# Kernel optimization log

Measured on AMD Instinct MI355X. Metric: run time of the kernel, lower is better.

The kernel has to match this reference:

```python
import jax, jax.numpy as jnp
import numpy as np

N_NODES = 100000
N_EDGES = 1200000
D_IN = 64
HID = 64
N_CLASSES = 3
N_GRAPHS = 128


def setup_inputs() -> dict:
    key = jax.random.key(0)
    ks = jax.random.split(key, 16)
    def lin(k, fan_in, fan_out):
        s = 1.0 / np.sqrt(fan_in)
        return jax.random.uniform(k, (fan_in, fan_out), jnp.float32, -s, s)
    x = jax.random.normal(ks[0], (N_NODES, D_IN), jnp.float32)
    edge_index = jax.random.randint(ks[1], (2, N_EDGES), 0, N_NODES, jnp.int64 if jax.config.jax_enable_x64 else jnp.int32).astype(jnp.int32)
    batch = jnp.sort(jax.random.randint(ks[2], (N_NODES,), 0, N_GRAPHS).astype(jnp.int32))
    return {
        "x": x,
        "edge_index": edge_index,
        "batch": batch,
        # GraphConv l: out = segment_sum(x[src]) @ Wr + br + x @ Ws  (lin_rel has bias, lin_root no bias)
        "Wr1": lin(ks[3], D_IN, HID), "br1": jnp.zeros((HID,), jnp.float32), "Ws1": lin(ks[4], D_IN, HID),
        "Wr2": lin(ks[5], HID, HID), "br2": jnp.zeros((HID,), jnp.float32), "Ws2": lin(ks[6], HID, HID),
        "Wr3": lin(ks[7], HID, HID), "br3": jnp.zeros((HID,), jnp.float32), "Ws3": lin(ks[8], HID, HID),
        "W_fc1": lin(ks[9], HID, HID), "b_fc1": jnp.zeros((HID,), jnp.float32),
        "W_fc2": lin(ks[10], HID, N_CLASSES), "b_fc2": jnp.zeros((N_CLASSES,), jnp.float32),
    }


def _graph_conv(x, src, dst, Wr, br, Ws):
    # gather -> scatter-add aggregate -> two linear transforms (PyG GraphConv, aggr='add')
    agg = jax.ops.segment_sum(x[src], dst, num_segments=N_NODES)  # [N, d]
    return agg @ Wr + br + x @ Ws


def reference(x, edge_index, batch, Wr1, br1, Ws1, Wr2, br2, Ws2, Wr3, br3, Ws3, W_fc1, b_fc1, W_fc2, b_fc2):
    src, dst = edge_index[0], edge_index[1]
    h = jax.nn.relu(_graph_conv(x, src, dst, Wr1, br1, Ws1))  # dropout is identity at inference
    h = jax.nn.relu(_graph_conv(h, src, dst, Wr2, br2, Ws2))
    h = jax.nn.relu(_graph_conv(h, src, dst, Wr3, br3, Ws3))
    g = jax.ops.segment_sum(h, batch, num_segments=N_GRAPHS)  # global_add_pool -> [G, H]
    g = jax.nn.relu(g @ W_fc1 + b_fc1)
    logits = g @ W_fc2 + b_fc2
    return jax.nn.log_softmax(logits, axis=-1)
```

## Files before the change

kernel.cpp:

```cpp
#include <hip/hip_runtime.h>

#define N_NODES   100000
#define N_EDGES   1200000
#define D         64
#define N_GRAPHS  128
#define N_CLASSES 3

#define TILE      64
#define NTILES    ((N_NODES + TILE - 1) / TILE)
#define TCAP      1024
#define ASTRIDE   72

#define EPB       8192
#define NEB       ((N_EDGES + EPB - 1) / EPB)
#define GRID_PB   1024

typedef unsigned int  uint;
typedef unsigned short ushort;
typedef __attribute__((ext_vector_type(8))) short bf16x8;
typedef __attribute__((ext_vector_type(4))) float f32x4;

__device__ __forceinline__ ushort bf16_rne(float f) {
    uint u = __float_as_uint(f);
    u += 0x7FFFu + ((u >> 16) & 1u);
    return (ushort)(u >> 16);
}
__device__ __forceinline__ float bf16f(ushort h) {
    return __uint_as_float((uint)h << 16);
}
__device__ __forceinline__ void acc8(float* a, uint4 v) {
    a[0] += __uint_as_float(v.x << 16);
    a[1] += __uint_as_float(v.x & 0xFFFF0000u);
    a[2] += __uint_as_float(v.y << 16);
    a[3] += __uint_as_float(v.y & 0xFFFF0000u);
    a[4] += __uint_as_float(v.z << 16);
    a[5] += __uint_as_float(v.z & 0xFFFF0000u);
    a[6] += __uint_as_float(v.w << 16);
    a[7] += __uint_as_float(v.w & 0xFFFF0000u);
}

template<typename PT>
__device__ __forceinline__ void gather_idx(
        float* acc, PT cp, int len,
        const ushort* __restrict__ hin, int fq8) {
    int j = 0;
    for (; j + 8 <= len; j += 8) {
        int s0 = cp[j + 0], s1 = cp[j + 1], s2 = cp[j + 2], s3 = cp[j + 3];
        int s4 = cp[j + 4], s5 = cp[j + 5], s6 = cp[j + 6], s7 = cp[j + 7];
        uint4 v0 = *(const uint4*)(hin + (size_t)s0 * D + fq8);
        uint4 v1 = *(const uint4*)(hin + (size_t)s1 * D + fq8);
        uint4 v2 = *(const uint4*)(hin + (size_t)s2 * D + fq8);
        uint4 v3 = *(const uint4*)(hin + (size_t)s3 * D + fq8);
        uint4 v4 = *(const uint4*)(hin + (size_t)s4 * D + fq8);
        uint4 v5 = *(const uint4*)(hin + (size_t)s5 * D + fq8);
        uint4 v6 = *(const uint4*)(hin + (size_t)s6 * D + fq8);
        uint4 v7 = *(const uint4*)(hin + (size_t)s7 * D + fq8);
        acc8(acc, v0); acc8(acc, v1); acc8(acc, v2); acc8(acc, v3);
        acc8(acc, v4); acc8(acc, v5); acc8(acc, v6); acc8(acc, v7);
    }
    for (; j + 4 <= len; j += 4) {
        int s0 = cp[j + 0], s1 = cp[j + 1], s2 = cp[j + 2], s3 = cp[j + 3];
        uint4 v0 = *(const uint4*)(hin + (size_t)s0 * D + fq8);
        uint4 v1 = *(const uint4*)(hin + (size_t)s1 * D + fq8);
        uint4 v2 = *(const uint4*)(hin + (size_t)s2 * D + fq8);
        uint4 v3 = *(const uint4*)(hin + (size_t)s3 * D + fq8);
        acc8(acc, v0); acc8(acc, v1); acc8(acc, v2); acc8(acc, v3);
    }
    for (; j < len; ++j) {
        uint4 v = *(const uint4*)(hin + (size_t)cp[j] * D + fq8);
        acc8(acc, v);
    }
}

__device__ __forceinline__ void store_agg_bf16(ushort* aggB, int ln, int fq8, const float* acc) {
    uint4 o;
    o.x = (uint)bf16_rne(acc[0]) | ((uint)bf16_rne(acc[1]) << 16);
    o.y = (uint)bf16_rne(acc[2]) | ((uint)bf16_rne(acc[3]) << 16);
    o.z = (uint)bf16_rne(acc[4]) | ((uint)bf16_rne(acc[5]) << 16);
    o.w = (uint)bf16_rne(acc[6]) | ((uint)bf16_rne(acc[7]) << 16);
    *(uint4*)&aggB[ln * ASTRIDE + fq8] = o;
}

__device__ __forceinline__ void mfma_gemm(
        const ushort* __restrict__ hin,
        const ushort* aggB,
        const ushort* __restrict__ Bp,
        int node0, int tid, f32x4* acc) {
    const int lane = tid & 63;
    const int w    = tid >> 6;
    const int r16  = lane & 15;
    const int khi  = lane >> 4;
#pragma unroll
    for (int mt = 0; mt < 4; ++mt) acc[mt] = (f32x4){0.f, 0.f, 0.f, 0.f};
    const ushort* bp = Bp + (w * 64 + lane) * 8;
#pragma unroll
    for (int st = 0; st < 4; ++st) {
        bf16x8 bhi = *(const bf16x8*)(bp + (2 * st    ) * 2048);
        bf16x8 blo = *(const bf16x8*)(bp + (2 * st + 1) * 2048);
        if (st < 2) {
#pragma unroll
            for (int mt = 0; mt < 4; ++mt) {
                bf16x8 a = *(const bf16x8*)(aggB + (16 * mt + r16) * ASTRIDE + st * 32 + khi * 8);
                acc[mt] = __builtin_amdgcn_mfma_f32_16x16x32_bf16(a, bhi, acc[mt], 0, 0, 0);
                acc[mt] = __builtin_amdgcn_mfma_f32_16x16x32_bf16(a, blo, acc[mt], 0, 0, 0);
            }
        } else {
#pragma unroll
            for (int mt = 0; mt < 4; ++mt) {
                bf16x8 a = *(const bf16x8*)(hin + (size_t)(node0 + 16 * mt + r16) * D
                                                + (st - 2) * 32 + khi * 8);
                acc[mt] = __builtin_amdgcn_mfma_f32_16x16x32_bf16(a, bhi, acc[mt], 0, 0, 0);
                acc[mt] = __builtin_amdgcn_mfma_f32_16x16x32_bf16(a, blo, acc[mt], 0, 0, 0);
            }
        }
    }
}

__global__ __launch_bounds__(256) void prep_binA_kernel(
        const float* __restrict__ x, ushort* __restrict__ Xb,
        const int* __restrict__ src, const int* __restrict__ dst,
        int* __restrict__ gcur, int* __restrict__ cbuf,
        const float* __restrict__ Wr1, const float* __restrict__ Ws1,
        const float* __restrict__ Wr2, const float* __restrict__ Ws2,
        const float* __restrict__ Wr3, const float* __restrict__ Ws3,
        ushort* __restrict__ Bp) {
    __shared__ int hist[NTILES];
    __shared__ int pos[NTILES];
    const int tid = threadIdx.x;
    const int bid = blockIdx.x;

    if (bid < NEB) {
        const int e0 = bid * EPB;
        int e1 = e0 + EPB; if (e1 > N_EDGES) e1 = N_EDGES;
        for (int i = tid; i < NTILES; i += 256) hist[i] = 0;
        __syncthreads();
        for (int e = e0 + tid; e < e1; e += 256)
            atomicAdd(&hist[dst[e] >> 6], 1);
        __syncthreads();
        for (int b = tid; b < NTILES; b += 256)
            pos[b] = hist[b] ? atomicAdd(&gcur[b], hist[b]) : 0;
        __syncthreads();
        for (int e = e0 + tid; e < e1; e += 256) {
            int d = dst[e];
            int b = d >> 6;
            int r = atomicAdd(&pos[b], 1);
            if (r < TCAP) cbuf[b * TCAP + r] = src[e] | ((d & 63) << 17);
        }
    } else {
        const int cb  = bid - NEB;
        const int NCB = GRID_PB - NEB;
        const int nodeF4 = N_NODES * D / 4;
        for (int i = cb * 256 + tid; i < nodeF4; i += NCB * 256) {
            float4 v = ((const float4*)x)[i];
            ushort4 o;
            o.x = bf16_rne(v.x); o.y = bf16_rne(v.y);
            o.z = bf16_rne(v.z); o.w = bf16_rne(v.w);
            ((ushort4*)Xb)[i] = o;
        }
        for (int it = cb * 256 + tid; it < 3 * 8 * 4 * 64; it += NCB * 256) {
            int l  = it & 63;
            int w  = (it >> 6) & 3;
            int kt = (it >> 8) & 7;
            int ly = it >> 11;
            int st = kt >> 1;
            int col = w * 16 + (l & 15);
            int kb  = (st & 1) * 32 + (l >> 4) * 8;
            const float* W = (st < 2) ? (ly == 0 ? Wr1 : ly == 1 ? Wr2 : Wr3)
                                      : (ly == 0 ? Ws1 : ly == 1 ? Ws2 : Ws3);
            ushort o[8];
#pragma unroll
            for (int j = 0; j < 8; ++j) {
                float v = W[(kb + j) * D + col];
                ushort h = bf16_rne(v);
                if (kt & 1) {
                    float r = v - bf16f(h);
                    h = bf16_rne(r);
                }
                o[j] = h;
            }
            uint4 u;
            u.x = (uint)o[0] | ((uint)o[1] << 16);
            u.y = (uint)o[2] | ((uint)o[3] << 16);
            u.z = (uint)o[4] | ((uint)o[5] << 16);
            u.w = (uint)o[6] | ((uint)o[7] << 16);
            *(uint4*)(Bp + (size_t)ly * 16384 + ((kt * 4 + w) * 64 + l) * 8) = u;
        }
    }
}

__global__ __launch_bounds__(256, 6) void layer1_fused_kernel(
        const ushort* __restrict__ hin,
        const int* __restrict__ gcur,
        const int* __restrict__ cbuf,
        int* __restrict__ csr,
        int2* __restrict__ rptr2,
        const ushort* __restrict__ Bp,
        const float* __restrict__ br,
        ushort* __restrict__ hout) {
    __shared__ int    ebuf[TCAP];
    __shared__ int    sortedS[TCAP];
    __shared__ ushort aggB[TILE * ASTRIDE];
    __shared__ int    ldeg[TILE];
    __shared__ int    lbeg[TILE];
    __shared__ int    lcur[TILE];

    const int tid   = threadIdx.x;
    const int tile  = blockIdx.x;
    const int base  = tile * TCAP;
    const int node0 = tile * TILE;

    int E = gcur[tile]; if (E > TCAP) E = TCAP;
    if (tid < TILE) ldeg[tid] = 0;
    for (int i = tid; i < E; i += 256) ebuf[i] = cbuf[base + i];
    __syncthreads();

    for (int i = tid; i < E; i += 256)
        atomicAdd(&ldeg[(ebuf[i] >> 17) & 63], 1);
    __syncthreads();

    if (tid < TILE) {
        int v = ldeg[tid];
        int s = v;
        for (int off = 1; off < 64; off <<= 1) {
            int u = __shfl_up(s, off, 64);
            if (tid >= off) s += u;
        }
        int beg = s - v;
        lbeg[tid] = beg;
        lcur[tid] = beg;
        int n = node0 + tid;
        if (n < N_NODES) rptr2[n] = make_int2(base + beg, base + beg + v);
    }
    __syncthreads();

    for (int i = tid; i < E; i += 256) {
        int p  = ebuf[i];
        int ld = (p >> 17) & 63;
        int s  = p & 0x1FFFF;
        int q  = atomicAdd(&lcur[ld], 1);
        sortedS[q]    = s;
        csr[base + q] = s;
    }
    __syncthreads();

    const int fq8 = (tid & 7) * 8;
    for (int r = 0; r < 2; ++r) {
        int ln = r * 32 + (tid >> 3);
        int n  = node0 + ln;
        float acc[8] = {0.f, 0.f, 0.f, 0.f, 0.f, 0.f, 0.f, 0.f};
        if (n < N_NODES)
            gather_idx(acc, (const int*)&sortedS[lbeg[ln]], ldeg[ln], hin, fq8);
        store_agg_bf16(aggB, ln, fq8, acc);
    }
    __syncthreads();

    f32x4 acc[4];
    mfma_gemm(hin, aggB, Bp, node0, tid, acc);

    const int lane = tid & 63;
    const int col  = (tid >> 6) * 16 + (lane & 15);
    const int khi  = lane >> 4;
    const float bias = br[col];
#pragma unroll
    for (int mt = 0; mt < 4; ++mt) {
#pragma unroll
        for (int i = 0; i < 4; ++i) {
            int n = node0 + 16 * mt + khi * 4 + i;
            if (n < N_NODES)
                hout[(size_t)n * D + col] = bf16_rne(fmaxf(acc[mt][i] + bias, 0.f));
        }
    }
}

template<int DO_POOL>
__global__ __launch_bounds__(256, 6) void fused_layer_kernel(
        const ushort* __restrict__ hin,
        const int2* __restrict__ rptr2,
        const int* __restrict__ csr,
        const ushort* __restrict__ Bp,
        const float* __restrict__ br,
        ushort* __restrict__ hout,
        const int* __restrict__ batch,
        float* __restrict__ g) {
    __shared__ ushort aggB[TILE * ASTRIDE];
    __shared__ int    bS[TILE];

    const int tid   = threadIdx.x;
    const int node0 = blockIdx.x * TILE;

    if (DO_POOL && tid < TILE) {
        int n = node0 + tid;
        bS[tid] = (n < N_NODES) ? batch[n] : -1;
    }

    const int fq8 = (tid & 7) * 8;
    for (int r = 0; r < 2; ++r) {
        int ln = r * 32 + (tid >> 3);
        int n  = node0 + ln;
        float acc[8] = {0.f, 0.f, 0.f, 0.f, 0.f, 0.f, 0.f, 0.f};
        if (n < N_NODES) {
            int2 be = rptr2[n];
            gather_idx(acc, csr + be.x, be.y - be.x, hin, fq8);
        }
        store_agg_bf16(aggB, ln, fq8, acc);
    }
    __syncthreads();

    f32x4 acc[4];
    mfma_gemm(hin, aggB, Bp, node0, tid, acc);

    const int lane = tid & 63;
    const int col  = (tid >> 6) * 16 + (lane & 15);
    const int khi  = lane >> 4;
    const float bias = br[col];

    if (!DO_POOL) {
#pragma unroll
        for (int mt = 0; mt < 4; ++mt) {
#pragma unroll
            for (int i = 0; i < 4; ++i) {
                int n = node0 + 16 * mt + khi * 4 + i;
                if (n < N_NODES)
                    hout[(size_t)n * D + col] = bf16_rne(fmaxf(acc[mt][i] + bias, 0.f));
            }
        }
    } else {
        __syncthreads();
#pragma unroll
        for (int mt = 0; mt < 4; ++mt) {
#pragma unroll
            for (int i = 0; i < 4; ++i) {
                float v = fmaxf(acc[mt][i] + bias, 0.f);
                aggB[(16 * mt + khi * 4 + i) * ASTRIDE + col] = bf16_rne(v);
            }
        }
        __syncthreads();
        int f    = tid & 63;
        int part = tid >> 6;
        int ln0  = part * 16;
        int cur  = bS[ln0];
        float acc2 = 0.f;
        for (int ln = ln0; ln < ln0 + 16; ++ln) {
            int b = bS[ln];
            if (b < 0) break;
            if (b != cur) {
                atomicAdd(&g[cur * D + f], acc2);
                acc2 = 0.f;
                cur = b;
            }
            acc2 += bf16f(aggB[ln * ASTRIDE + f]);
        }
        if (cur >= 0) atomicAdd(&g[cur * D + f], acc2);
    }
}

__global__ __launch_bounds__(64) void head_kernel(
        const float* __restrict__ g,
        const float* __restrict__ Wfc1, const float* __restrict__ bfc1,
        const float* __restrict__ Wfc2, const float* __restrict__ bfc2,
        float* __restrict__ out) {
    __shared__ float hS[D];
    __shared__ float lS[N_CLASSES];
    int gr = blockIdx.x;
    int f  = threadIdx.x;

    float acc = bfc1[f];
#pragma unroll
    for (int k = 0; k < D; ++k) acc += g[gr * D + k] * Wfc1[k * D + f];
    hS[f] = fmaxf(acc, 0.f);
    __syncthreads();

    if (f < N_CLASSES) {
        float a = bfc2[f];
#pragma unroll
        for (int k = 0; k < D; ++k) a += hS[k] * Wfc2[k * N_CLASSES + f];
        lS[f] = a;
    }
    __syncthreads();

    if (f == 0) {
        float m = fmaxf(lS[0], fmaxf(lS[1], lS[2]));
        float s = expf(lS[0] - m) + expf(lS[1] - m) + expf(lS[2] - m);
        float lse = m + logf(s);
        out[gr * 3 + 0] = lS[0] - lse;
        out[gr * 3 + 1] = lS[1] - lse;
        out[gr * 3 + 2] = lS[2] - lse;
    }
}

extern "C" void kernel_launch(void* const* d_in, const int* in_sizes, int n_in,
                              void* d_out, int out_size, void* d_ws, size_t ws_size,
                              hipStream_t stream) {
    const float* x     = (const float*)d_in[0];
    const int*   edge  = (const int*)d_in[1];
    const int*   batch = (const int*)d_in[2];
    const float* Wr1 = (const float*)d_in[3];
    const float* br1 = (const float*)d_in[4];
    const float* Ws1 = (const float*)d_in[5];
    const float* Wr2 = (const float*)d_in[6];
    const float* br2 = (const float*)d_in[7];
    const float* Ws2 = (const float*)d_in[8];
    const float* Wr3 = (const float*)d_in[9];
    const float* br3 = (const float*)d_in[10];
    const float* Ws3 = (const float*)d_in[11];
    const float* Wfc1 = (const float*)d_in[12];
    const float* bfc1 = (const float*)d_in[13];
    const float* Wfc2 = (const float*)d_in[14];
    const float* bfc2 = (const float*)d_in[15];

    const int* src = edge;
    const int* dst = edge + N_EDGES;

    ushort* Xb     = (ushort*)d_ws;
    ushort* Ab     = Xb + (size_t)N_NODES * D;
    float*  g      = (float*)(Ab + (size_t)N_NODES * D);
    int*   gcur    = (int*)(g + (size_t)N_GRAPHS * D);
    int2*  rptr2   = (int2*)(gcur + 1564);
    int*   cbuf    = (int*)(rptr2 + N_NODES);
    int*   csr     = cbuf + (size_t)NTILES * TCAP;
    ushort* Bp     = (ushort*)(csr + (size_t)NTILES * TCAP);

    dim3 blk256(256);
    dim3 grdT((int)NTILES);

    hipMemsetAsync(g, 0, (size_t)(N_GRAPHS * D + 1564) * sizeof(float), stream);

    prep_binA_kernel<<<dim3(GRID_PB), blk256, 0, stream>>>(
        x, Xb, src, dst, gcur, cbuf, Wr1, Ws1, Wr2, Ws2, Wr3, Ws3, Bp);

    layer1_fused_kernel<<<grdT, blk256, 0, stream>>>(Xb, gcur, cbuf, csr, rptr2,
                                                     Bp, br1, Ab);

    fused_layer_kernel<0><<<grdT, blk256, 0, stream>>>(Ab, rptr2, csr, Bp + 16384, br2, Xb, batch, g);
    fused_layer_kernel<1><<<grdT, blk256, 0, stream>>>(Xb, rptr2, csr, Bp + 32768, br3, Ab, batch, g);

    head_kernel<<<dim3(N_GRAPHS), dim3(64), 0, stream>>>(g, Wfc1, bfc1, Wfc2, bfc2, (float*)d_out);
}
```

Measured before the change: 258.1 us.

## Degree-sort nodes within tiles for gather balance; vectorize edge binning loads

Within each 64-node tile, nodes are ranked by in-degree and the gather loop visits them in sorted order. Nodes of similar degree then share a wavefront, which cuts divergence from uneven neighbor counts. The binning pass now reads dst/src as int4 and halves edges per block to raise parallelism. The cost is an O(64) rank loop per node plus an extra barrier. The int4 loads assume EPB stays a multiple of 4 and the arrays are aligned.

```diff
diff --git a/kernel.cpp b/kernel.cpp
--- a/kernel.cpp
+++ b/kernel.cpp
@@ -11,7 +11,7 @@
 #define TCAP      1024
 #define ASTRIDE   72
 
-#define EPB       8192
+#define EPB       4096
 #define NEB       ((N_EDGES + EPB - 1) / EPB)
 #define GRID_PB   1024
 
@@ -134,17 +134,28 @@
         int e1 = e0 + EPB; if (e1 > N_EDGES) e1 = N_EDGES;
         for (int i = tid; i < NTILES; i += 256) hist[i] = 0;
         __syncthreads();
-        for (int e = e0 + tid; e < e1; e += 256)
-            atomicAdd(&hist[dst[e] >> 6], 1);
+        for (int e = e0 + tid * 4; e < e1; e += 1024) {
+            int4 d4 = *(const int4*)(dst + e);
+            atomicAdd(&hist[d4.x >> 6], 1);
+            atomicAdd(&hist[d4.y >> 6], 1);
+            atomicAdd(&hist[d4.z >> 6], 1);
+            atomicAdd(&hist[d4.w >> 6], 1);
+        }
         __syncthreads();
         for (int b = tid; b < NTILES; b += 256)
             pos[b] = hist[b] ? atomicAdd(&gcur[b], hist[b]) : 0;
         __syncthreads();
-        for (int e = e0 + tid; e < e1; e += 256) {
-            int d = dst[e];
-            int b = d >> 6;
-            int r = atomicAdd(&pos[b], 1);
-            if (r < TCAP) cbuf[b * TCAP + r] = src[e] | ((d & 63) << 17);
+        for (int e = e0 + tid * 4; e < e1; e += 1024) {
+            int4 d4 = *(const int4*)(dst + e);
+            int4 s4 = *(const int4*)(src + e);
+#pragma unroll
+            for (int k = 0; k < 4; ++k) {
+                int d = (k == 0) ? d4.x : (k == 1) ? d4.y : (k == 2) ? d4.z : d4.w;
+                int s = (k == 0) ? s4.x : (k == 1) ? s4.y : (k == 2) ? s4.z : s4.w;
+                int b = d >> 6;
+                int r = atomicAdd(&pos[b], 1);
+                if (r < TCAP) cbuf[b * TCAP + r] = s | ((d & 63) << 17);
+            }
         }
     } else {
         const int cb  = bid - NEB;
@@ -203,6 +214,7 @@
     __shared__ int    ldeg[TILE];
     __shared__ int    lbeg[TILE];
     __shared__ int    lcur[TILE];
+    __shared__ unsigned char permS[TILE];
 
     const int tid   = threadIdx.x;
     const int tile  = blockIdx.x;
@@ -230,6 +242,12 @@
         lcur[tid] = beg;
         int n = node0 + tid;
         if (n < N_NODES) rptr2[n] = make_int2(base + beg, base + beg + v);
+        int rnk = 0;
+        for (int j = 0; j < TILE; ++j) {
+            int dj = ldeg[j];
+            rnk += (dj < v) || (dj == v && j < tid);
+        }
+        permS[rnk] = (unsigned char)tid;
     }
     __syncthreads();
 
@@ -245,10 +263,9 @@
 
     const int fq8 = (tid & 7) * 8;
     for (int r = 0; r < 2; ++r) {
-        int ln = r * 32 + (tid >> 3);
-        int n  = node0 + ln;
+        int ln = permS[r * 32 + (tid >> 3)];
         float acc[8] = {0.f, 0.f, 0.f, 0.f, 0.f, 0.f, 0.f, 0.f};
-        if (n < N_NODES)
+        if (ldeg[ln] > 0)
             gather_idx(acc, (const int*)&sortedS[lbeg[ln]], ldeg[ln], hin, fq8);
         store_agg_bf16(aggB, ln, fq8, acc);
     }
@@ -284,24 +301,38 @@
         float* __restrict__ g) {
     __shared__ ushort aggB[TILE * ASTRIDE];
     __shared__ int    bS[TILE];
+    __shared__ int    begS[TILE];
+    __shared__ int    degS[TILE];
+    __shared__ unsigned char permS[TILE];
 
     const int tid   = threadIdx.x;
     const int node0 = blockIdx.x * TILE;
 
-    if (DO_POOL && tid < TILE) {
+    if (tid < TILE) {
         int n = node0 + tid;
-        bS[tid] = (n < N_NODES) ? batch[n] : -1;
-    }
+        if (DO_POOL) bS[tid] = (n < N_NODES) ? batch[n] : -1;
+        int2 be = (n < N_NODES) ? rptr2[n] : make_int2(0, 0);
+        begS[tid] = be.x;
+        degS[tid] = be.y - be.x;
+    }
+    __syncthreads();
+    if (tid < TILE) {
+        int d = degS[tid];
+        int rnk = 0;
+        for (int j = 0; j < TILE; ++j) {
+            int dj = degS[j];
+            rnk += (dj < d) || (dj == d && j < tid);
+        }
+        permS[rnk] = (unsigned char)tid;
+    }
+    __syncthreads();
 
     const int fq8 = (tid & 7) * 8;
     for (int r = 0; r < 2; ++r) {
-        int ln = r * 32 + (tid >> 3);
-        int n  = node0 + ln;
+        int ln = permS[r * 32 + (tid >> 3)];
         float acc[8] = {0.f, 0.f, 0.f, 0.f, 0.f, 0.f, 0.f, 0.f};
-        if (n < N_NODES) {
-            int2 be = rptr2[n];
-            gather_idx(acc, csr + be.x, be.y - be.x, hin, fq8);
-        }
+        if (degS[ln] > 0)
+            gather_idx(acc, csr + begS[ln], degS[ln], hin, fq8);
         store_agg_bf16(aggB, ln, fq8, acc);
     }
     __syncthreads();
```

Measured after the change: 250.4 us. 3.0% less time.
